# Kernel optimization log

Hardware: AMD Instinct MI355X
Metric: run time of the kernel (lower is better)

## Reference

```python
import jax, jax.numpy as jnp
import numpy as np

B, S, D, H = 2, 2048, 2048, 16
HD = D // H  # head_dim = 128
ROPE_BASE = 10000.0


def _rope_interleaved(x, cos, sin):
    # x: [B, S, H, HD]; cos/sin: [S, HD//2]
    xe = x[..., 0::2]
    xo = x[..., 1::2]
    c = cos[None, :, None, :]
    s = sin[None, :, None, :]
    oe = xe * c - xo * s
    oo = xe * s + xo * c
    # re-interleave pairs back to last dim
    return jnp.stack([oe, oo], axis=-1).reshape(x.shape)


def setup_inputs() -> dict:
    key = jax.random.key(0)
    k0, k1, k2, k3 = jax.random.split(key, 4)
    scale = D ** -0.5
    x = jax.random.normal(k0, (B, S, D), dtype=jnp.float32)
    wqk = jax.random.normal(k1, (2 * D, D), dtype=jnp.float32) * scale
    wv = jax.random.normal(k2, (D, D), dtype=jnp.float32) * scale
    wo = jax.random.normal(k3, (D, D), dtype=jnp.float32) * scale
    return {"x": x, "wqk": wqk, "wv": wv, "wo": wo}


def reference(x, wqk, wv, wo):
    b, s, d = x.shape
    # fused QK projection -> [B, S, 2, H, HD]
    xqk = (x @ wqk.T).reshape(b, s, 2, H, HD)
    xq = xqk[:, :, 0]
    xk = xqk[:, :, 1]
    xv = (x @ wv.T).reshape(b, s, H, HD)

    # interleaved rotary embedding (seqlen_offset=0, no-cache path)
    inv_freq = 1.0 / (ROPE_BASE ** (jnp.arange(0, HD, 2, dtype=jnp.float32) / HD))
    freqs = jnp.arange(s, dtype=jnp.float32)[:, None] * inv_freq[None, :]  # [S, HD//2]
    cos, sin = jnp.cos(freqs), jnp.sin(freqs)
    xq = _rope_interleaved(xq, cos, sin)
    xk = _rope_interleaved(xk, cos, sin)

    # causal scaled-dot-product attention
    scores = jnp.einsum("bqhd,bkhd->bhqk", xq, xk) * (HD ** -0.5)
    causal = jnp.tril(jnp.ones((s, s), dtype=bool))
    scores = jnp.where(causal[None, None], scores, jnp.finfo(scores.dtype).min)
    probs = jax.nn.softmax(scores, axis=-1)
    out = jnp.einsum("bhqk,bkhd->bqhd", probs, xv).reshape(b, s, d)
    return out @ wo.T
```

## Files before the change

kernel.cpp:

```cpp
#include <hip/hip_runtime.h>
#include <hip/hip_bf16.h>

#define NB 2
#define SEQ 2048
#define DMODEL 2048
#define NH 16
#define HD 128
#define QSCALE (0.08838834764831845f * 1.44269504088896f)
#define THRL2 11.5f

using bf16x8 = __attribute__((ext_vector_type(8))) __bf16;
using f32x4  = __attribute__((ext_vector_type(4))) float;

#define MFMA16 __builtin_amdgcn_mfma_f32_16x16x32_bf16

typedef __attribute__((address_space(1))) const void* gptr_t;
typedef __attribute__((address_space(3))) void* lptr_t;

__device__ inline void gload_lds16(const unsigned short* g, unsigned short* l) {
    __builtin_amdgcn_global_load_lds((gptr_t)g, (lptr_t)l, 16, 0, 0);
}

__device__ inline unsigned short f2b(float f) {
    unsigned u = __builtin_bit_cast(unsigned, f);
    u += 0x7FFF + ((u >> 16) & 1);
    return (unsigned short)(u >> 16);
}
__device__ inline float b2f(unsigned short h) {
    return __builtin_bit_cast(float, (unsigned)h << 16);
}
__device__ inline float fexp2(float x) {
    float r;
    asm("v_exp_f32 %0, %1" : "=v"(r) : "v"(x));
    return r;
}
__device__ inline unsigned cvtpk(float a, float b) {
    unsigned r;
    asm("v_cvt_pk_bf16_f32 %0, %1, %2" : "=v"(r) : "v"(a), "v"(b));
    return r;
}

__global__ void cast_f2b(const float* __restrict__ src, unsigned short* __restrict__ dst, int n) {
    int i = (blockIdx.x * 256 + threadIdx.x) * 4;
    if (i + 3 < n) {
        float4 v = *reinterpret_cast<const float4*>(src + i);
        ushort4 o;
        o.x = f2b(v.x); o.y = f2b(v.y); o.z = f2b(v.z); o.w = f2b(v.w);
        *reinterpret_cast<ushort4*>(dst + i) = o;
    }
}

template<int OUT_BF16>
__global__ __launch_bounds__(512) void gemm8p(const unsigned short* __restrict__ A,
                                              const unsigned short* __restrict__ Bw,
                                              void* __restrict__ Cout,
                                              int M, int N, int K) {
    __shared__ __align__(16) char lds[98304];
    int tid = threadIdx.x;
    int lane = tid & 63;
    int wid = tid >> 6;
    int wm = wid >> 2, wn = wid & 3;
    int row0 = blockIdx.y * 128;
    int col0 = blockIdx.x * 256;
    int lr = lane & 15, g = lane >> 4;

    const unsigned short* srcA[2];
    const unsigned short* srcB[4];
#pragma unroll
    for (int i = 0; i < 2; i++) {
        int chunk = i * 512 + tid;
        int ksub = chunk >> 9;
        int cw = chunk & 511;
        int row = cw >> 2, c = cw & 3;
        int cs = c ^ ((row >> 1) & 3);
        srcA[i] = A + (size_t)(row0 + row) * K + ksub * 32 + cs * 8;
    }
#pragma unroll
    for (int i = 0; i < 4; i++) {
        int chunk = i * 512 + tid;
        int ksub = chunk >> 10;
        int cw = chunk & 1023;
        int row = cw >> 2, c = cw & 3;
        int cs = c ^ ((row >> 1) & 3);
        srcB[i] = Bw + (size_t)(col0 + row) * K + ksub * 32 + cs * 8;
    }

    int offA[4][2], offB[4][2];
#pragma unroll
    for (int i = 0; i < 4; i++) {
        int row = wm * 64 + i * 16 + lr;
#pragma unroll
        for (int ks = 0; ks < 2; ks++)
            offA[i][ks] = ks * 8192 + row * 64 + ((g ^ ((row >> 1) & 3)) * 16);
    }
#pragma unroll
    for (int j = 0; j < 4; j++) {
        int row = wn * 64 + j * 16 + lr;
#pragma unroll
        for (int ks = 0; ks < 2; ks++)
            offB[j][ks] = ks * 16384 + row * 64 + ((g ^ ((row >> 1) & 3)) * 16);
    }

    f32x4 acc[4][4] = {};
    int NT = K >> 6;

#define STAGE8(t) {                                                                   \
        int kb_ = (t) * 64;                                                           \
        int bs_ = ((t) & 1) * 49152;                                                  \
        _Pragma("unroll")                                                             \
        for (int i_ = 0; i_ < 2; i_++)                                                \
            gload_lds16(srcA[i_] + kb_,                                               \
                (unsigned short*)(lds + bs_ + (i_ * 512 + (tid & ~63)) * 16));        \
        _Pragma("unroll")                                                             \
        for (int i_ = 0; i_ < 4; i_++)                                                \
            gload_lds16(srcB[i_] + kb_,                                               \
                (unsigned short*)(lds + bs_ + 16384 + (i_ * 512 + (tid & ~63)) * 16)); \
    }

    STAGE8(0);
    for (int t = 0; t < NT; ++t) {
        if (t + 1 < NT) {
            STAGE8(t + 1);
            asm volatile("s_waitcnt vmcnt(6)" ::: "memory");
        } else {
            asm volatile("s_waitcnt vmcnt(0)" ::: "memory");
        }
        __builtin_amdgcn_s_barrier();
        __builtin_amdgcn_sched_barrier(0);

        const char* ab = lds + (t & 1) * 49152;
        const char* bb = ab + 16384;

        bf16x8 b[4][2], a[2][2];
#pragma unroll
        for (int j = 0; j < 4; j++)
#pragma unroll
            for (int ks = 0; ks < 2; ks++)
                b[j][ks] = *reinterpret_cast<const bf16x8*>(bb + offB[j][ks]);
#pragma unroll
        for (int i = 0; i < 2; i++)
#pragma unroll
            for (int ks = 0; ks < 2; ks++)
                a[i][ks] = *reinterpret_cast<const bf16x8*>(ab + offA[i][ks]);
        asm volatile("s_waitcnt lgkmcnt(0)" ::: "memory");
        __builtin_amdgcn_sched_barrier(0);
        __builtin_amdgcn_s_setprio(1);
#pragma unroll
        for (int ks = 0; ks < 2; ks++)
#pragma unroll
            for (int i = 0; i < 2; i++)
#pragma unroll
                for (int j = 0; j < 4; j++)
                    acc[i][j] = MFMA16(a[i][ks], b[j][ks], acc[i][j], 0, 0, 0);
        __builtin_amdgcn_s_setprio(0);

        bf16x8 a2[2][2];
#pragma unroll
        for (int i = 0; i < 2; i++)
#pragma unroll
            for (int ks = 0; ks < 2; ks++)
                a2[i][ks] = *reinterpret_cast<const bf16x8*>(ab + offA[2 + i][ks]);
        asm volatile("s_waitcnt lgkmcnt(0)" ::: "memory");
        __builtin_amdgcn_sched_barrier(0);
        __builtin_amdgcn_s_barrier();
        __builtin_amdgcn_sched_barrier(0);
        __builtin_amdgcn_s_setprio(1);
#pragma unroll
        for (int ks = 0; ks < 2; ks++)
#pragma unroll
            for (int i = 0; i < 2; i++)
#pragma unroll
                for (int j = 0; j < 4; j++)
                    acc[2 + i][j] = MFMA16(a2[i][ks], b[j][ks], acc[2 + i][j], 0, 0, 0);
        __builtin_amdgcn_s_setprio(0);
    }
#undef STAGE8

    int orow = g * 4;
#pragma unroll
    for (int i = 0; i < 4; i++) {
#pragma unroll
        for (int j = 0; j < 4; j++) {
            int r0 = row0 + wm * 64 + i * 16 + orow;
            int c  = col0 + wn * 64 + j * 16 + lr;
#pragma unroll
            for (int r = 0; r < 4; r++) {
                float v = acc[i][j][r];
                if (OUT_BF16)
                    ((unsigned short*)Cout)[(size_t)(r0 + r) * N + c] = f2b(v);
                else
                    ((float*)Cout)[(size_t)(r0 + r) * N + c] = v;
            }
        }
    }
}

__global__ void rope_qk(const unsigned short* __restrict__ qkv,
                        unsigned short* __restrict__ qb,
                        unsigned short* __restrict__ kb) {
    int idx = blockIdx.x * 256 + threadIdx.x;
    int i = idx & 63;
    int h = (idx >> 6) & 15;
    int t = idx >> 10;
    int s = t & (SEQ - 1);
    int b = t >> 11;

    float inv = exp2f(-13.287712379549449f * (float)i * (1.0f / 64.0f));
    float ang = (float)s * inv;
    float sn, cs;
    sincosf(ang, &sn, &cs);

    const unsigned short* base = qkv + (size_t)t * 6144 + h * 128 + 2 * i;
    unsigned qv = *reinterpret_cast<const unsigned*>(base);
    unsigned kv = *reinterpret_cast<const unsigned*>(base + 2048);

    float qe = b2f((unsigned short)(qv & 0xFFFF));
    float qo = b2f((unsigned short)(qv >> 16));
    float ke = b2f((unsigned short)(kv & 0xFFFF));
    float ko = b2f((unsigned short)(kv >> 16));

    float qe2 = (qe * cs - qo * sn) * QSCALE;
    float qo2 = (qe * sn + qo * cs) * QSCALE;
    float ke2 = ke * cs - ko * sn;
    float ko2 = ke * sn + ko * cs;

    size_t o = ((size_t)(b * NH + h) * SEQ + s) * HD + 2 * i;
    *reinterpret_cast<unsigned*>(qb + o) = (unsigned)f2b(qe2) | ((unsigned)f2b(qo2) << 16);
    *reinterpret_cast<unsigned*>(kb + o) = (unsigned)f2b(ke2) | ((unsigned)f2b(ko2) << 16);
}

__global__ void v_rearr(const unsigned short* __restrict__ qkv, unsigned short* __restrict__ vt) {
    int idx = blockIdx.x * 256 + threadIdx.x;
    int s4 = (idx & 511) * 4;
    int d  = (idx >> 9) & 127;
    int h  = (idx >> 16) & 15;
    int b  = idx >> 20;
    ushort4 o;
    size_t rbase = (size_t)(b * SEQ + s4) * 6144 + 4096 + h * 128 + d;
    o.x = qkv[rbase];
    o.y = qkv[rbase + 6144];
    o.z = qkv[rbase + 2 * 6144];
    o.w = qkv[rbase + 3 * 6144];
    *reinterpret_cast<ushort4*>(vt + ((size_t)(b * NH + h) * HD + d) * SEQ + s4) = o;
}

__global__ __launch_bounds__(64, 1) void attn6(const unsigned short* __restrict__ Q,
                                               const unsigned short* __restrict__ Kb,
                                               const unsigned short* __restrict__ Vt,
                                               unsigned short* __restrict__ O) {
    __shared__ __align__(16) char lds[36864];

    int lane = threadIdx.x;
    int bid = blockIdx.x;
    int p  = bid >> 5;
    int bh = bid & 31;
    int lr = lane & 15;
    int g  = lane >> 4;
    int g4 = g * 4;
    int lk = g * 8;

    const unsigned short* Qp = Q  + (size_t)bh * SEQ * HD;
    const unsigned short* Kp = Kb + (size_t)bh * SEQ * HD;
    const unsigned short* Vp = Vt + (size_t)bh * HD * SEQ;
    char* pl = lds + 32768;
    int b = bh >> 4;
    int h = bh & 15;

    int srcoff[16];
#pragma unroll
    for (int i2 = 0; i2 < 16; ++i2) {
        int r = i2 * 4 + g;
        srcoff[i2] = r * HD + ((lr ^ (r & 7)) * 8);
    }

#define STAGEK(bufbase, kvbase)                                                     \
    {                                                                               \
        const unsigned short* kbase = Kp + (size_t)(kvbase) * HD;                   \
        _Pragma("unroll")                                                           \
        for (int i2 = 0; i2 < 16; ++i2)                                             \
            gload_lds16(kbase + srcoff[i2],                                         \
                        (unsigned short*)(lds + (bufbase) + i2 * 1024));            \
    }

    for (int ph = 0; ph < 2; ++ph) {
        int j  = ph ? (63 - p) : p;
        int q0 = j * 32;
        int ktiles = (j >> 1) + 1;

        bf16x8 qf[2][4];
#pragma unroll
        for (int f = 0; f < 2; f++)
#pragma unroll
            for (int kb = 0; kb < 4; kb++)
                qf[f][kb] = *reinterpret_cast<const bf16x8*>(Qp + (size_t)(q0 + f * 16 + lr) * HD + kb * 32 + lk);

        f32x4 oacc[2][8] = {};
        float m[2] = { -1e30f, -1e30f }, l[2] = { 0.0f, 0.0f };
        int qrow[2] = { q0 + lr, q0 + 16 + lr };

        STAGEK(0, 0);

        int cur = 0;
        for (int t = 0; t < ktiles; ++t) {
            int kv0 = t * 64;
            if (t + 1 < ktiles) {
                STAGEK((cur ^ 1) * 16384, kv0 + 64);
                asm volatile("s_waitcnt vmcnt(16)" ::: "memory");
            } else {
                asm volatile("s_waitcnt vmcnt(0)" ::: "memory");
            }
            __builtin_amdgcn_sched_barrier(0);

            char* kb_c = lds + cur * 16384;
            f32x4 s[2][4] = {};
#pragma unroll
            for (int kb = 0; kb < 4; kb++) {
#pragma unroll
                for (int jj = 0; jj < 4; jj++) {
                    int row = jj * 16 + lr;
                    int cin = ((kb * 4 + g) ^ (row & 7));
                    bf16x8 kf = *reinterpret_cast<const bf16x8*>(kb_c + row * 256 + cin * 16);
                    s[0][jj] = MFMA16(kf, qf[0][kb], s[0][jj], 0, 0, 0);
                    s[1][jj] = MFMA16(kf, qf[1][kb], s[1][jj], 0, 0, 0);
                }
            }

            bf16x8 vf[8][2];
#pragma unroll
            for (int db = 0; db < 8; db++)
#pragma unroll
                for (int ks = 0; ks < 2; ks++)
                    vf[db][ks] = *reinterpret_cast<const bf16x8*>(Vp + (size_t)(db * 16 + lr) * SEQ + kv0 + ks * 32 + lk);

#pragma unroll
            for (int f = 0; f < 2; f++) {
                int q = qrow[f];
                bool full = (kv0 + 63 <= q0 + f * 16);
                float mx = -1e30f;
                if (full) {
#pragma unroll
                    for (int jj = 0; jj < 4; jj++)
#pragma unroll
                        for (int r = 0; r < 4; r++)
                            mx = fmaxf(mx, s[f][jj][r]);
                } else {
#pragma unroll
                    for (int jj = 0; jj < 4; jj++)
#pragma unroll
                        for (int r = 0; r < 4; r++) {
                            int kv = kv0 + jj * 16 + g4 + r;
                            float v = (kv <= q) ? s[f][jj][r] : -1e30f;
                            s[f][jj][r] = v;
                            mx = fmaxf(mx, v);
                        }
                }
                mx = fmaxf(mx, __shfl_xor(mx, 16));
                mx = fmaxf(mx, __shfl_xor(mx, 32));

                if (!__all(mx <= m[f] + THRL2)) {
                    float mn = fmaxf(m[f], mx);
                    float sc = fexp2(m[f] - mn);
                    m[f] = mn;
                    l[f] *= sc;
#pragma unroll
                    for (int db = 0; db < 8; db++)
#pragma unroll
                        for (int r = 0; r < 4; r++)
                            oacc[f][db][r] *= sc;
                }

                int row = f * 16 + lr;
                int rb = row * 128;
                int sw = (row & 7) << 4;
                float rs = 0.0f;
#pragma unroll
                for (int jj = 0; jj < 4; jj++)
#pragma unroll
                    for (int hh = 0; hh < 2; hh++) {
                        float p0 = fexp2(s[f][jj][2 * hh]     - m[f]);
                        float p1 = fexp2(s[f][jj][2 * hh + 1] - m[f]);
                        rs += p0 + p1;
                        unsigned pk = cvtpk(p0, p1);
                        int colb = jj * 32 + g * 8 + 4 * hh;
                        *reinterpret_cast<unsigned*>(pl + rb + (colb ^ sw)) = pk;
                    }
                rs += __shfl_xor(rs, 16);
                rs += __shfl_xor(rs, 32);
                l[f] += rs;
            }

            asm volatile("s_waitcnt lgkmcnt(0)" ::: "memory");
            __builtin_amdgcn_sched_barrier(0);

            bf16x8 pb[2][2];
#pragma unroll
            for (int f = 0; f < 2; f++)
#pragma unroll
                for (int ks = 0; ks < 2; ks++) {
                    int row = f * 16 + lr;
                    int off = row * 128 + ((ks * 64 + g * 16) ^ ((row & 7) << 4));
                    pb[f][ks] = *reinterpret_cast<const bf16x8*>(pl + off);
                }
#pragma unroll
            for (int db = 0; db < 8; db++)
#pragma unroll
                for (int ks = 0; ks < 2; ks++) {
                    oacc[0][db] = MFMA16(vf[db][ks], pb[0][ks], oacc[0][db], 0, 0, 0);
                    oacc[1][db] = MFMA16(vf[db][ks], pb[1][ks], oacc[1][db], 0, 0, 0);
                }

            cur ^= 1;
        }

#pragma unroll
        for (int f = 0; f < 2; f++) {
            float inv = 1.0f / l[f];
            int q = q0 + f * 16 + lr;
            unsigned short* op = O + ((size_t)(b * SEQ + q)) * DMODEL + h * HD;
#pragma unroll
            for (int db = 0; db < 8; db++) {
                ushort4 o4;
                o4.x = f2b(oacc[f][db][0] * inv);
                o4.y = f2b(oacc[f][db][1] * inv);
                o4.z = f2b(oacc[f][db][2] * inv);
                o4.w = f2b(oacc[f][db][3] * inv);
                *reinterpret_cast<ushort4*>(op + db * 16 + g4) = o4;
            }
        }
    }
#undef STAGEK
}

extern "C" void kernel_launch(void* const* d_in, const int* in_sizes, int n_in,
                              void* d_out, int out_size, void* d_ws, size_t ws_size,
                              hipStream_t stream) {
    const float* x   = (const float*)d_in[0];
    const float* wqk = (const float*)d_in[1];
    const float* wv  = (const float*)d_in[2];
    const float* wo  = (const float*)d_in[3];

    unsigned short* xb  = (unsigned short*)d_ws;
    unsigned short* wb  = xb  + (size_t)8388608;
    unsigned short* qkv = wb  + (size_t)16777216;
    unsigned short* qb  = qkv + (size_t)25165824;
    unsigned short* kb  = qb  + (size_t)8388608;
    unsigned short* vt  = kb  + (size_t)8388608;
    unsigned short* ao  = vt  + (size_t)8388608;

    cast_f2b<<<8192, 256, 0, stream>>>(x,   xb, 8388608);
    cast_f2b<<<8192, 256, 0, stream>>>(wqk, wb, 8388608);
    cast_f2b<<<4096, 256, 0, stream>>>(wv,  wb + 8388608, 4194304);
    cast_f2b<<<4096, 256, 0, stream>>>(wo,  wb + 12582912, 4194304);

    gemm8p<1><<<dim3(24, 32), 512, 0, stream>>>(xb, wb, (void*)qkv, 4096, 6144, 2048);

    rope_qk<<<16384, 256, 0, stream>>>(qkv, qb, kb);
    v_rearr<<<8192, 256, 0, stream>>>(qkv, vt);

    attn6<<<1024, 64, 0, stream>>>(qb, kb, vt, ao);

    gemm8p<0><<<dim3(8, 32), 512, 0, stream>>>(ao, wb + 12582912, d_out, 4096, 2048, 2048);
}
```

Measured before the change: 316.6 us.

## Use 256x256-tile GEMM kernel with split-phase pipelining for QKV projection

Adds a new GEMM kernel with 256x256 output tiles (128 KB LDS, double-buffered, 8 waves each computing 128x64) and uses it for the fused QKV projection in place of the 128x256 tile kernel. The larger tile raises arithmetic intensity and cuts global/L2 traffic per FLOP. Loads for the next K-step are interleaved with MFMA phases and separated by barriers, with wave priority raised around the MFMA blocks. In exchange, the grid shrinks to 384 blocks with one block per CU because of the LDS size, and each thread holds more accumulator registers.

```diff
diff --git a/kernel.cpp b/kernel.cpp
--- a/kernel.cpp
+++ b/kernel.cpp
@@ -47,6 +47,170 @@
         ushort4 o;
         o.x = f2b(v.x); o.y = f2b(v.y); o.z = f2b(v.z); o.w = f2b(v.w);
         *reinterpret_cast<ushort4*>(dst + i) = o;
+    }
+}
+
+template<int OUT_BF16>
+__global__ __launch_bounds__(512) void gemm256(const unsigned short* __restrict__ A,
+                                               const unsigned short* __restrict__ Bw,
+                                               void* __restrict__ Cout,
+                                               int M, int N, int K) {
+    __shared__ __align__(16) char lds[131072];
+    int tid = threadIdx.x;
+    int lane = tid & 63;
+    int wid = tid >> 6;
+    int wm = wid >> 2, wn = wid & 3;
+    int row0 = blockIdx.y * 256;
+    int col0 = blockIdx.x * 256;
+    int lr = lane & 15, g = lane >> 4;
+
+    const unsigned short *pA[2], *pB[2];
+    int ldsc[2];
+#pragma unroll
+    for (int i = 0; i < 2; i++) {
+        int chunk = i * 512 + tid;
+        int row = chunk >> 2, c = chunk & 3;
+        int cs = c ^ ((row >> 1) & 3);
+        pA[i] = A  + (size_t)(row0 + row) * K + cs * 8;
+        pB[i] = Bw + (size_t)(col0 + row) * K + cs * 8;
+        ldsc[i] = (i * 512 + (tid & ~63)) * 16;
+    }
+
+#define STAGE_A(bufb, kbase, h)  {                                                    \
+        _Pragma("unroll")                                                             \
+        for (int i_ = 0; i_ < 2; i_++)                                                \
+            gload_lds16(pA[i_] + (kbase) + (h) * 32,                                  \
+                (unsigned short*)(lds + (bufb) + (h) * 16384 + ldsc[i_]));            \
+    }
+#define STAGE_B(bufb, kbase, h)  {                                                    \
+        _Pragma("unroll")                                                             \
+        for (int i_ = 0; i_ < 2; i_++)                                                \
+            gload_lds16(pB[i_] + (kbase) + (h) * 32,                                  \
+                (unsigned short*)(lds + (bufb) + 32768 + (h) * 16384 + ldsc[i_]));    \
+    }
+
+    int offA[8][2], offB[4][2];
+#pragma unroll
+    for (int i = 0; i < 8; i++) {
+        int row = wm * 128 + i * 16 + lr;
+#pragma unroll
+        for (int ks = 0; ks < 2; ks++)
+            offA[i][ks] = ks * 16384 + row * 64 + ((g ^ ((row >> 1) & 3)) * 16);
+    }
+#pragma unroll
+    for (int j = 0; j < 4; j++) {
+        int row = wn * 64 + j * 16 + lr;
+#pragma unroll
+        for (int ks = 0; ks < 2; ks++)
+            offB[j][ks] = 32768 + ks * 16384 + row * 64 + ((g ^ ((row >> 1) & 3)) * 16);
+    }
+
+    f32x4 acc[8][4] = {};
+    int NT = K >> 6;
+
+    STAGE_A(0, 0, 0); STAGE_B(0, 0, 0); STAGE_A(0, 0, 1); STAGE_B(0, 0, 1);
+    asm volatile("s_waitcnt vmcnt(4)" ::: "memory");
+    __builtin_amdgcn_s_barrier();
+    __builtin_amdgcn_sched_barrier(0);
+
+    for (int t = 0; t < NT; ++t) {
+        const char* bufc = lds + (t & 1) * 65536;
+        int bufn = ((t + 1) & 1) * 65536;
+        bool hn = (t + 1 < NT);
+        int kn = (t + 1) * 64;
+
+        bf16x8 av[4], bv[4];
+
+#pragma unroll
+        for (int j = 0; j < 4; j++) bv[j] = *reinterpret_cast<const bf16x8*>(bufc + offB[j][0]);
+#pragma unroll
+        for (int i = 0; i < 4; i++) av[i] = *reinterpret_cast<const bf16x8*>(bufc + offA[i][0]);
+        if (hn) STAGE_A(bufn, kn, 0);
+        __builtin_amdgcn_s_barrier();
+        asm volatile("s_waitcnt lgkmcnt(0)" ::: "memory");
+        __builtin_amdgcn_sched_barrier(0);
+        __builtin_amdgcn_s_setprio(1);
+#pragma unroll
+        for (int i = 0; i < 4; i++)
+#pragma unroll
+            for (int j = 0; j < 4; j++)
+                acc[i][j] = MFMA16(av[i], bv[j], acc[i][j], 0, 0, 0);
+        __builtin_amdgcn_s_setprio(0);
+        __builtin_amdgcn_s_barrier();
+        __builtin_amdgcn_sched_barrier(0);
+
+#pragma unroll
+        for (int i = 0; i < 4; i++) av[i] = *reinterpret_cast<const bf16x8*>(bufc + offA[4 + i][0]);
+        if (hn) STAGE_B(bufn, kn, 0);
+        __builtin_amdgcn_s_barrier();
+        asm volatile("s_waitcnt lgkmcnt(0)" ::: "memory");
+        __builtin_amdgcn_sched_barrier(0);
+        __builtin_amdgcn_s_setprio(1);
+#pragma unroll
+        for (int i = 0; i < 4; i++)
+#pragma unroll
+            for (int j = 0; j < 4; j++)
+                acc[4 + i][j] = MFMA16(av[i], bv[j], acc[4 + i][j], 0, 0, 0);
+        __builtin_amdgcn_s_setprio(0);
+        if (hn) asm volatile("s_waitcnt vmcnt(4)" ::: "memory");
+        else    asm volatile("s_waitcnt vmcnt(0)" ::: "memory");
+        __builtin_amdgcn_s_barrier();
+        __builtin_amdgcn_sched_barrier(0);
+
+#pragma unroll
+        for (int j = 0; j < 4; j++) bv[j] = *reinterpret_cast<const bf16x8*>(bufc + offB[j][1]);
+#pragma unroll
+        for (int i = 0; i < 4; i++) av[i] = *reinterpret_cast<const bf16x8*>(bufc + offA[i][1]);
+        if (hn) STAGE_A(bufn, kn, 1);
+        __builtin_amdgcn_s_barrier();
+        asm volatile("s_waitcnt lgkmcnt(0)" ::: "memory");
+        __builtin_amdgcn_sched_barrier(0);
+        __builtin_amdgcn_s_setprio(1);
+#pragma unroll
+        for (int i = 0; i < 4; i++)
+#pragma unroll
+            for (int j = 0; j < 4; j++)
+                acc[i][j] = MFMA16(av[i], bv[j], acc[i][j], 0, 0, 0);
+        __builtin_amdgcn_s_setprio(0);
+        __builtin_amdgcn_s_barrier();
+        __builtin_amdgcn_sched_barrier(0);
+
+#pragma unroll
+        for (int i = 0; i < 4; i++) av[i] = *reinterpret_cast<const bf16x8*>(bufc + offA[4 + i][1]);
+        if (hn) STAGE_B(bufn, kn, 1);
+        __builtin_amdgcn_s_barrier();
+        asm volatile("s_waitcnt lgkmcnt(0)" ::: "memory");
+        __builtin_amdgcn_sched_barrier(0);
+        __builtin_amdgcn_s_setprio(1);
+#pragma unroll
+        for (int i = 0; i < 4; i++)
+#pragma unroll
+            for (int j = 0; j < 4; j++)
+                acc[4 + i][j] = MFMA16(av[i], bv[j], acc[4 + i][j], 0, 0, 0);
+        __builtin_amdgcn_s_setprio(0);
+        if (hn) asm volatile("s_waitcnt vmcnt(4)" ::: "memory");
+        __builtin_amdgcn_s_barrier();
+        __builtin_amdgcn_sched_barrier(0);
+    }
+#undef STAGE_A
+#undef STAGE_B
+
+    int orow = g * 4;
+#pragma unroll
+    for (int i = 0; i < 8; i++) {
+#pragma unroll
+        for (int j = 0; j < 4; j++) {
+            int r0 = row0 + wm * 128 + i * 16 + orow;
+            int c  = col0 + wn * 64 + j * 16 + lr;
+#pragma unroll
+            for (int r = 0; r < 4; r++) {
+                float v = acc[i][j][r];
+                if (OUT_BF16)
+                    ((unsigned short*)Cout)[(size_t)(r0 + r) * N + c] = f2b(v);
+                else
+                    ((float*)Cout)[(size_t)(r0 + r) * N + c] = v;
+            }
+        }
     }
 }
 
@@ -452,7 +616,7 @@
     cast_f2b<<<4096, 256, 0, stream>>>(wv,  wb + 8388608, 4194304);
     cast_f2b<<<4096, 256, 0, stream>>>(wo,  wb + 12582912, 4194304);
 
-    gemm8p<1><<<dim3(24, 32), 512, 0, stream>>>(xb, wb, (void*)qkv, 4096, 6144, 2048);
+    gemm256<1><<<dim3(24, 16), 512, 0, stream>>>(xb, wb, (void*)qkv, 4096, 6144, 2048);
 
     rope_qk<<<16384, 256, 0, stream>>>(qkv, qb, kb);
     v_rearr<<<8192, 256, 0, stream>>>(qkv, vt);
```

Measured after the change: 332.0 us. 1.05x slower.

## Split KV tiles across two waves per query tile with LDS merge

Applied to the files above, without the earlier changes.

Replaces the single-wave attention kernel, which processed a paired short and long query tile in sequence, with a two-wave block per query tile. Each wave handles alternating KV tiles with its own K buffer and P scratch, and the two partial softmax states are merged through LDS at the end. The grid doubles to 2048 blocks and blocks are issued longest-first. This aims to raise parallelism and shorten the serial KV loop, at the cost of losing the double-buffered K prefetch within a wave and adding a merge step with barriers.

```diff
diff --git a/kernel.cpp b/kernel.cpp
--- a/kernel.cpp
+++ b/kernel.cpp
@@ -244,16 +244,20 @@
     *reinterpret_cast<ushort4*>(vt + ((size_t)(b * NH + h) * HD + d) * SEQ + s4) = o;
 }
 
-__global__ __launch_bounds__(64, 1) void attn6(const unsigned short* __restrict__ Q,
-                                               const unsigned short* __restrict__ Kb,
-                                               const unsigned short* __restrict__ Vt,
-                                               unsigned short* __restrict__ O) {
-    __shared__ __align__(16) char lds[36864];
-
-    int lane = threadIdx.x;
+__global__ __launch_bounds__(128, 1) void attn7(const unsigned short* __restrict__ Q,
+                                                const unsigned short* __restrict__ Kb,
+                                                const unsigned short* __restrict__ Vt,
+                                                unsigned short* __restrict__ O) {
+    __shared__ __align__(16) char lds[40960];
+
+    int tid = threadIdx.x;
+    int lane = tid & 63;
+    int w = tid >> 6;
     int bid = blockIdx.x;
-    int p  = bid >> 5;
+    int qt = 63 - (bid >> 5);
     int bh = bid & 31;
+    int q0 = qt * 32;
+    int ktiles = (qt >> 1) + 1;
     int lr = lane & 15;
     int g  = lane >> 4;
     int g4 = g * 4;
@@ -262,7 +266,8 @@
     const unsigned short* Qp = Q  + (size_t)bh * SEQ * HD;
     const unsigned short* Kp = Kb + (size_t)bh * SEQ * HD;
     const unsigned short* Vp = Vt + (size_t)bh * HD * SEQ;
-    char* pl = lds + 32768;
+    char* kl = lds + w * 16384;
+    char* pl = lds + 32768 + w * 4096;
     int b = bh >> 4;
     int h = bh & 15;
 
@@ -273,162 +278,167 @@
         srcoff[i2] = r * HD + ((lr ^ (r & 7)) * 8);
     }
 
-#define STAGEK(bufbase, kvbase)                                                     \
-    {                                                                               \
+#define STAGEK7(kvbase) {                                                           \
         const unsigned short* kbase = Kp + (size_t)(kvbase) * HD;                   \
         _Pragma("unroll")                                                           \
         for (int i2 = 0; i2 < 16; ++i2)                                             \
             gload_lds16(kbase + srcoff[i2],                                         \
-                        (unsigned short*)(lds + (bufbase) + i2 * 1024));            \
-    }
-
-    for (int ph = 0; ph < 2; ++ph) {
-        int j  = ph ? (63 - p) : p;
-        int q0 = j * 32;
-        int ktiles = (j >> 1) + 1;
-
-        bf16x8 qf[2][4];
+                        (unsigned short*)(kl + i2 * 1024));                         \
+    }
+
+    bf16x8 qf[2][4];
+#pragma unroll
+    for (int f = 0; f < 2; f++)
+#pragma unroll
+        for (int kb = 0; kb < 4; kb++)
+            qf[f][kb] = *reinterpret_cast<const bf16x8*>(Qp + (size_t)(q0 + f * 16 + lr) * HD + kb * 32 + lk);
+
+    f32x4 oacc[2][8] = {};
+    float m[2] = { -1e30f, -1e30f }, l[2] = { 0.0f, 0.0f };
+    int qrow[2] = { q0 + lr, q0 + 16 + lr };
+
+    if (w < ktiles) STAGEK7(w * 64);
+
+    for (int t = w; t < ktiles; t += 2) {
+        int kv0 = t * 64;
+        asm volatile("s_waitcnt vmcnt(0)" ::: "memory");
+        __builtin_amdgcn_sched_barrier(0);
+
+        f32x4 s[2][4] = {};
+#pragma unroll
+        for (int kb = 0; kb < 4; kb++) {
+#pragma unroll
+            for (int jj = 0; jj < 4; jj++) {
+                int row = jj * 16 + lr;
+                int cin = ((kb * 4 + g) ^ (row & 7));
+                bf16x8 kf = *reinterpret_cast<const bf16x8*>(kl + row * 256 + cin * 16);
+                s[0][jj] = MFMA16(kf, qf[0][kb], s[0][jj], 0, 0, 0);
+                s[1][jj] = MFMA16(kf, qf[1][kb], s[1][jj], 0, 0, 0);
+            }
+        }
+
+        bf16x8 vf[8][2];
+#pragma unroll
+        for (int db = 0; db < 8; db++)
+#pragma unroll
+            for (int ks = 0; ks < 2; ks++)
+                vf[db][ks] = *reinterpret_cast<const bf16x8*>(Vp + (size_t)(db * 16 + lr) * SEQ + kv0 + ks * 32 + lk);
+
+#pragma unroll
+        for (int f = 0; f < 2; f++) {
+            int q = qrow[f];
+            bool full = (kv0 + 63 <= q0 + f * 16);
+            float mx = -1e30f;
+            if (full) {
+#pragma unroll
+                for (int jj = 0; jj < 4; jj++)
+#pragma unroll
+                    for (int r = 0; r < 4; r++)
+                        mx = fmaxf(mx, s[f][jj][r]);
+            } else {
+#pragma unroll
+                for (int jj = 0; jj < 4; jj++)
+#pragma unroll
+                    for (int r = 0; r < 4; r++) {
+                        int kv = kv0 + jj * 16 + g4 + r;
+                        float v = (kv <= q) ? s[f][jj][r] : -1e30f;
+                        s[f][jj][r] = v;
+                        mx = fmaxf(mx, v);
+                    }
+            }
+            mx = fmaxf(mx, __shfl_xor(mx, 16));
+            mx = fmaxf(mx, __shfl_xor(mx, 32));
+
+            if (!__all(mx <= m[f] + THRL2)) {
+                float mn = fmaxf(m[f], mx);
+                float sc = fexp2(m[f] - mn);
+                m[f] = mn;
+                l[f] *= sc;
+#pragma unroll
+                for (int db = 0; db < 8; db++)
+#pragma unroll
+                    for (int r = 0; r < 4; r++)
+                        oacc[f][db][r] *= sc;
+            }
+
+            int row = f * 16 + lr;
+            int rb = row * 128;
+            int sw = (row & 7) << 4;
+            float rs = 0.0f;
+#pragma unroll
+            for (int jj = 0; jj < 4; jj++)
+#pragma unroll
+                for (int hh = 0; hh < 2; hh++) {
+                    float p0 = fexp2(s[f][jj][2 * hh]     - m[f]);
+                    float p1 = fexp2(s[f][jj][2 * hh + 1] - m[f]);
+                    rs += p0 + p1;
+                    unsigned pk = cvtpk(p0, p1);
+                    int colb = jj * 32 + g * 8 + 4 * hh;
+                    *reinterpret_cast<unsigned*>(pl + rb + (colb ^ sw)) = pk;
+                }
+            rs += __shfl_xor(rs, 16);
+            rs += __shfl_xor(rs, 32);
+            l[f] += rs;
+        }
+
+        asm volatile("s_waitcnt lgkmcnt(0)" ::: "memory");
+        __builtin_amdgcn_sched_barrier(0);
+
+        if (t + 2 < ktiles) STAGEK7((t + 2) * 64);
+
+        bf16x8 pb[2][2];
 #pragma unroll
         for (int f = 0; f < 2; f++)
 #pragma unroll
-            for (int kb = 0; kb < 4; kb++)
-                qf[f][kb] = *reinterpret_cast<const bf16x8*>(Qp + (size_t)(q0 + f * 16 + lr) * HD + kb * 32 + lk);
-
-        f32x4 oacc[2][8] = {};
-        float m[2] = { -1e30f, -1e30f }, l[2] = { 0.0f, 0.0f };
-        int qrow[2] = { q0 + lr, q0 + 16 + lr };
-
-        STAGEK(0, 0);
-
-        int cur = 0;
-        for (int t = 0; t < ktiles; ++t) {
-            int kv0 = t * 64;
-            if (t + 1 < ktiles) {
-                STAGEK((cur ^ 1) * 16384, kv0 + 64);
-                asm volatile("s_waitcnt vmcnt(16)" ::: "memory");
-            } else {
-                asm volatile("s_waitcnt vmcnt(0)" ::: "memory");
-            }
-            __builtin_amdgcn_sched_barrier(0);
-
-            char* kb_c = lds + cur * 16384;
-            f32x4 s[2][4] = {};
-#pragma unroll
-            for (int kb = 0; kb < 4; kb++) {
-#pragma unroll
-                for (int jj = 0; jj < 4; jj++) {
-                    int row = jj * 16 + lr;
-                    int cin = ((kb * 4 + g) ^ (row & 7));
-                    bf16x8 kf = *reinterpret_cast<const bf16x8*>(kb_c + row * 256 + cin * 16);
-                    s[0][jj] = MFMA16(kf, qf[0][kb], s[0][jj], 0, 0, 0);
-                    s[1][jj] = MFMA16(kf, qf[1][kb], s[1][jj], 0, 0, 0);
-                }
-            }
-
-            bf16x8 vf[8][2];
+            for (int ks = 0; ks < 2; ks++) {
+                int row = f * 16 + lr;
+                int off = row * 128 + ((ks * 64 + g * 16) ^ ((row & 7) << 4));
+                pb[f][ks] = *reinterpret_cast<const bf16x8*>(pl + off);
+            }
+#pragma unroll
+        for (int db = 0; db < 8; db++)
+#pragma unroll
+            for (int ks = 0; ks < 2; ks++) {
+                oacc[0][db] = MFMA16(vf[db][ks], pb[0][ks], oacc[0][db], 0, 0, 0);
+                oacc[1][db] = MFMA16(vf[db][ks], pb[1][ks], oacc[1][db], 0, 0, 0);
+            }
+    }
+#undef STAGEK7
+
+    __syncthreads();
+    if (w == 1) {
+#pragma unroll
+        for (int f = 0; f < 2; f++) {
 #pragma unroll
             for (int db = 0; db < 8; db++)
-#pragma unroll
-                for (int ks = 0; ks < 2; ks++)
-                    vf[db][ks] = *reinterpret_cast<const bf16x8*>(Vp + (size_t)(db * 16 + lr) * SEQ + kv0 + ks * 32 + lk);
-
-#pragma unroll
-            for (int f = 0; f < 2; f++) {
-                int q = qrow[f];
-                bool full = (kv0 + 63 <= q0 + f * 16);
-                float mx = -1e30f;
-                if (full) {
-#pragma unroll
-                    for (int jj = 0; jj < 4; jj++)
-#pragma unroll
-                        for (int r = 0; r < 4; r++)
-                            mx = fmaxf(mx, s[f][jj][r]);
-                } else {
-#pragma unroll
-                    for (int jj = 0; jj < 4; jj++)
-#pragma unroll
-                        for (int r = 0; r < 4; r++) {
-                            int kv = kv0 + jj * 16 + g4 + r;
-                            float v = (kv <= q) ? s[f][jj][r] : -1e30f;
-                            s[f][jj][r] = v;
-                            mx = fmaxf(mx, v);
-                        }
-                }
-                mx = fmaxf(mx, __shfl_xor(mx, 16));
-                mx = fmaxf(mx, __shfl_xor(mx, 32));
-
-                if (!__all(mx <= m[f] + THRL2)) {
-                    float mn = fmaxf(m[f], mx);
-                    float sc = fexp2(m[f] - mn);
-                    m[f] = mn;
-                    l[f] *= sc;
-#pragma unroll
-                    for (int db = 0; db < 8; db++)
-#pragma unroll
-                        for (int r = 0; r < 4; r++)
-                            oacc[f][db][r] *= sc;
-                }
-
-                int row = f * 16 + lr;
-                int rb = row * 128;
-                int sw = (row & 7) << 4;
-                float rs = 0.0f;
-#pragma unroll
-                for (int jj = 0; jj < 4; jj++)
-#pragma unroll
-                    for (int hh = 0; hh < 2; hh++) {
-                        float p0 = fexp2(s[f][jj][2 * hh]     - m[f]);
-                        float p1 = fexp2(s[f][jj][2 * hh + 1] - m[f]);
-                        rs += p0 + p1;
-                        unsigned pk = cvtpk(p0, p1);
-                        int colb = jj * 32 + g * 8 + 4 * hh;
-                        *reinterpret_cast<unsigned*>(pl + rb + (colb ^ sw)) = pk;
-                    }
-                rs += __shfl_xor(rs, 16);
-                rs += __shfl_xor(rs, 32);
-                l[f] += rs;
-            }
-
-            asm volatile("s_waitcnt lgkmcnt(0)" ::: "memory");
-            __builtin_amdgcn_sched_barrier(0);
-
-            bf16x8 pb[2][2];
-#pragma unroll
-            for (int f = 0; f < 2; f++)
-#pragma unroll
-                for (int ks = 0; ks < 2; ks++) {
-                    int row = f * 16 + lr;
-                    int off = row * 128 + ((ks * 64 + g * 16) ^ ((row & 7) << 4));
-                    pb[f][ks] = *reinterpret_cast<const bf16x8*>(pl + off);
-                }
-#pragma unroll
-            for (int db = 0; db < 8; db++)
-#pragma unroll
-                for (int ks = 0; ks < 2; ks++) {
-                    oacc[0][db] = MFMA16(vf[db][ks], pb[0][ks], oacc[0][db], 0, 0, 0);
-                    oacc[1][db] = MFMA16(vf[db][ks], pb[1][ks], oacc[1][db], 0, 0, 0);
-                }
-
-            cur ^= 1;
-        }
-
+                *reinterpret_cast<f32x4*>(lds + ((f * 8 + db) * 64 + lane) * 16) = oacc[f][db];
+            *reinterpret_cast<float2*>(lds + 16384 + (f * 64 + lane) * 8) = make_float2(m[f], l[f]);
+        }
+    }
+    __syncthreads();
+    if (w == 0) {
 #pragma unroll
         for (int f = 0; f < 2; f++) {
-            float inv = 1.0f / l[f];
+            float2 ml1 = *reinterpret_cast<const float2*>(lds + 16384 + (f * 64 + lane) * 8);
+            float mt = fmaxf(m[f], ml1.x);
+            float sc0 = fexp2(m[f] - mt);
+            float sc1 = fexp2(ml1.x - mt);
+            float L = l[f] * sc0 + ml1.y * sc1;
+            float inv = 1.0f / L;
             int q = q0 + f * 16 + lr;
             unsigned short* op = O + ((size_t)(b * SEQ + q)) * DMODEL + h * HD;
 #pragma unroll
             for (int db = 0; db < 8; db++) {
+                f32x4 o1 = *reinterpret_cast<const f32x4*>(lds + ((f * 8 + db) * 64 + lane) * 16);
                 ushort4 o4;
-                o4.x = f2b(oacc[f][db][0] * inv);
-                o4.y = f2b(oacc[f][db][1] * inv);
-                o4.z = f2b(oacc[f][db][2] * inv);
-                o4.w = f2b(oacc[f][db][3] * inv);
+                o4.x = f2b((oacc[f][db][0] * sc0 + o1[0] * sc1) * inv);
+                o4.y = f2b((oacc[f][db][1] * sc0 + o1[1] * sc1) * inv);
+                o4.z = f2b((oacc[f][db][2] * sc0 + o1[2] * sc1) * inv);
+                o4.w = f2b((oacc[f][db][3] * sc0 + o1[3] * sc1) * inv);
                 *reinterpret_cast<ushort4*>(op + db * 16 + g4) = o4;
             }
         }
     }
-#undef STAGEK
 }
 
 extern "C" void kernel_launch(void* const* d_in, const int* in_sizes, int n_in,
@@ -457,7 +467,7 @@
     rope_qk<<<16384, 256, 0, stream>>>(qkv, qb, kb);
     v_rearr<<<8192, 256, 0, stream>>>(qkv, vt);
 
-    attn6<<<1024, 64, 0, stream>>>(qb, kb, vt, ao);
+    attn7<<<2048, 128, 0, stream>>>(qb, kb, vt, ao);
 
     gemm8p<0><<<dim3(8, 32), 512, 0, stream>>>(ao, wb + 12582912, d_out, 4096, 2048, 2048);
 }
```

Measured after the change: 326.2 us. 3.0% more time.

## Fuse RoPE and head-major Q/K scatter into QKV GEMM epilogue, tile V transpose

Applied to the files above, without the earlier changes.

The QKV projection GEMM epilogue now applies the rotary embedding, using a precomputed cos/sin table and a lane shuffle to fetch the pair partner, and writes Q (pre-scaled) and K straight into head-major bf16 buffers. This removes the separate rope_qk kernel and the round trip of the full QKV intermediate. V is written row-major and transposed by a new LDS-tiled kernel, replacing the strided per-element gather. The cost is a more complex epilogue with scattered 2-byte stores and table loads, plus one extra small kernel to build the table.

```diff
diff --git a/kernel.cpp b/kernel.cpp
--- a/kernel.cpp
+++ b/kernel.cpp
@@ -50,10 +50,25 @@
     }
 }
 
-template<int OUT_BF16>
+__global__ void rope_tab(float2* __restrict__ tab) {
+    int idx = blockIdx.x * 256 + threadIdx.x;
+    int i = idx & 63;
+    int s = idx >> 6;
+    float inv = exp2f(-13.287712379549449f * (float)i * (1.0f / 64.0f));
+    float ang = (float)s * inv;
+    float sn, cs;
+    sincosf(ang, &sn, &cs);
+    tab[idx] = make_float2(cs, sn);
+}
+
+template<int MODE>
 __global__ __launch_bounds__(512) void gemm8p(const unsigned short* __restrict__ A,
                                               const unsigned short* __restrict__ Bw,
                                               void* __restrict__ Cout,
+                                              unsigned short* __restrict__ qb,
+                                              unsigned short* __restrict__ kbp,
+                                              unsigned short* __restrict__ vx,
+                                              const float2* __restrict__ tab,
                                               int M, int N, int K) {
     __shared__ __align__(16) char lds[98304];
     int tid = threadIdx.x;
@@ -177,71 +192,87 @@
 #undef STAGE8
 
     int orow = g * 4;
-#pragma unroll
-    for (int i = 0; i < 4; i++) {
-#pragma unroll
-        for (int j = 0; j < 4; j++) {
-            int r0 = row0 + wm * 64 + i * 16 + orow;
-            int c  = col0 + wn * 64 + j * 16 + lr;
-#pragma unroll
-            for (int r = 0; r < 4; r++) {
-                float v = acc[i][j][r];
-                if (OUT_BF16)
-                    ((unsigned short*)Cout)[(size_t)(r0 + r) * N + c] = f2b(v);
-                else
-                    ((float*)Cout)[(size_t)(r0 + r) * N + c] = v;
+    if (MODE == 0) {
+#pragma unroll
+        for (int i = 0; i < 4; i++) {
+#pragma unroll
+            for (int j = 0; j < 4; j++) {
+                int r0 = row0 + wm * 64 + i * 16 + orow;
+                int c  = col0 + wn * 64 + j * 16 + lr;
+#pragma unroll
+                for (int r = 0; r < 4; r++)
+                    ((float*)Cout)[(size_t)(r0 + r) * N + c] = acc[i][j][r];
             }
         }
-    }
-}
-
-__global__ void rope_qk(const unsigned short* __restrict__ qkv,
-                        unsigned short* __restrict__ qb,
-                        unsigned short* __restrict__ kb) {
-    int idx = blockIdx.x * 256 + threadIdx.x;
-    int i = idx & 63;
-    int h = (idx >> 6) & 15;
-    int t = idx >> 10;
-    int s = t & (SEQ - 1);
-    int b = t >> 11;
-
-    float inv = exp2f(-13.287712379549449f * (float)i * (1.0f / 64.0f));
-    float ang = (float)s * inv;
-    float sn, cs;
-    sincosf(ang, &sn, &cs);
-
-    const unsigned short* base = qkv + (size_t)t * 6144 + h * 128 + 2 * i;
-    unsigned qv = *reinterpret_cast<const unsigned*>(base);
-    unsigned kv = *reinterpret_cast<const unsigned*>(base + 2048);
-
-    float qe = b2f((unsigned short)(qv & 0xFFFF));
-    float qo = b2f((unsigned short)(qv >> 16));
-    float ke = b2f((unsigned short)(kv & 0xFFFF));
-    float ko = b2f((unsigned short)(kv >> 16));
-
-    float qe2 = (qe * cs - qo * sn) * QSCALE;
-    float qo2 = (qe * sn + qo * cs) * QSCALE;
-    float ke2 = ke * cs - ko * sn;
-    float ko2 = ke * sn + ko * cs;
-
-    size_t o = ((size_t)(b * NH + h) * SEQ + s) * HD + 2 * i;
-    *reinterpret_cast<unsigned*>(qb + o) = (unsigned)f2b(qe2) | ((unsigned)f2b(qo2) << 16);
-    *reinterpret_cast<unsigned*>(kb + o) = (unsigned)f2b(ke2) | ((unsigned)f2b(ko2) << 16);
-}
-
-__global__ void v_rearr(const unsigned short* __restrict__ qkv, unsigned short* __restrict__ vt) {
-    int idx = blockIdx.x * 256 + threadIdx.x;
-    int s4 = (idx & 511) * 4;
-    int d  = (idx >> 9) & 127;
-    int h  = (idx >> 16) & 15;
-    int b  = idx >> 20;
-    ushort4 o;
-    size_t rbase = (size_t)(b * SEQ + s4) * 6144 + 4096 + h * 128 + d;
-    o.x = qkv[rbase];
-    o.y = qkv[rbase + 6144];
-    o.z = qkv[rbase + 2 * 6144];
-    o.w = qkv[rbase + 3 * 6144];
-    *reinterpret_cast<ushort4*>(vt + ((size_t)(b * NH + h) * HD + d) * SEQ + s4) = o;
+    } else {
+        int bx = blockIdx.x;
+        if (bx < 16) {
+            const bool isQ = (bx < 8);
+            unsigned short* dst = isQ ? qb : kbp;
+#pragma unroll
+            for (int i = 0; i < 4; i++) {
+#pragma unroll
+                for (int j = 0; j < 4; j++) {
+                    int c = col0 + wn * 64 + j * 16 + lr;
+                    int cc = c & 2047;
+                    int h = cc >> 7, d = cc & 127, i2 = d >> 1;
+                    int odd = lr & 1;
+#pragma unroll
+                    for (int r = 0; r < 4; r++) {
+                        int trow = row0 + wm * 64 + i * 16 + orow + r;
+                        int s = trow & (SEQ - 1), bb2 = trow >> 11;
+                        float v = acc[i][j][r];
+                        float pv = __shfl_xor(v, 1);
+                        float2 cssn = tab[s * 64 + i2];
+                        float out = odd ? (pv * cssn.y + v * cssn.x)
+                                        : (v * cssn.x - pv * cssn.y);
+                        if (isQ) out *= QSCALE;
+                        dst[((size_t)((bb2 * NH + h) * SEQ + s)) * HD + d] = f2b(out);
+                    }
+                }
+            }
+        } else {
+#pragma unroll
+            for (int i = 0; i < 4; i++) {
+#pragma unroll
+                for (int j = 0; j < 4; j++) {
+                    int cc = col0 + wn * 64 + j * 16 + lr - 4096;
+#pragma unroll
+                    for (int r = 0; r < 4; r++) {
+                        int trow = row0 + wm * 64 + i * 16 + orow + r;
+                        vx[(size_t)trow * 2048 + cc] = f2b(acc[i][j][r]);
+                    }
+                }
+            }
+        }
+    }
+}
+
+__global__ __launch_bounds__(256) void v_tr(const unsigned short* __restrict__ vx,
+                                            unsigned short* __restrict__ vt) {
+    __shared__ unsigned short tl[64][68];
+    int bid = blockIdx.x;
+    int st = bid & 31;
+    int dt = (bid >> 5) & 1;
+    int bh = bid >> 6;
+    int b = bh >> 4, h = bh & 15;
+    int tid = threadIdx.x;
+    int rr = tid >> 2;
+    int rc = (tid & 3) * 16;
+
+    const unsigned short* src = vx + (size_t)(b * SEQ + st * 64 + rr) * 2048 + h * HD + dt * 64 + rc;
+    uint4 v0 = *reinterpret_cast<const uint4*>(src);
+    uint4 v1 = *reinterpret_cast<const uint4*>(src + 8);
+    *reinterpret_cast<uint4*>(&tl[rr][rc]) = v0;
+    *reinterpret_cast<uint4*>(&tl[rr][rc + 8]) = v1;
+    __syncthreads();
+
+    unsigned short tmp[16];
+#pragma unroll
+    for (int k = 0; k < 16; k++) tmp[k] = tl[rc + k][rr];
+    unsigned short* dst = vt + (size_t)(bh * HD + dt * 64 + rr) * SEQ + st * 64 + rc;
+    *reinterpret_cast<uint4*>(dst)     = *reinterpret_cast<const uint4*>(&tmp[0]);
+    *reinterpret_cast<uint4*>(dst + 8) = *reinterpret_cast<const uint4*>(&tmp[8]);
 }
 
 __global__ __launch_bounds__(64, 1) void attn6(const unsigned short* __restrict__ Q,
@@ -441,23 +472,24 @@
 
     unsigned short* xb  = (unsigned short*)d_ws;
     unsigned short* wb  = xb  + (size_t)8388608;
-    unsigned short* qkv = wb  + (size_t)16777216;
-    unsigned short* qb  = qkv + (size_t)25165824;
+    unsigned short* qb  = wb  + (size_t)16777216;
     unsigned short* kb  = qb  + (size_t)8388608;
-    unsigned short* vt  = kb  + (size_t)8388608;
+    unsigned short* vx  = kb  + (size_t)8388608;
+    unsigned short* vt  = vx  + (size_t)8388608;
     unsigned short* ao  = vt  + (size_t)8388608;
+    float2* tab = (float2*)(ao + (size_t)8388608);
 
     cast_f2b<<<8192, 256, 0, stream>>>(x,   xb, 8388608);
     cast_f2b<<<8192, 256, 0, stream>>>(wqk, wb, 8388608);
     cast_f2b<<<4096, 256, 0, stream>>>(wv,  wb + 8388608, 4194304);
     cast_f2b<<<4096, 256, 0, stream>>>(wo,  wb + 12582912, 4194304);
-
-    gemm8p<1><<<dim3(24, 32), 512, 0, stream>>>(xb, wb, (void*)qkv, 4096, 6144, 2048);
-
-    rope_qk<<<16384, 256, 0, stream>>>(qkv, qb, kb);
-    v_rearr<<<8192, 256, 0, stream>>>(qkv, vt);
+    rope_tab<<<512, 256, 0, stream>>>(tab);
+
+    gemm8p<2><<<dim3(24, 32), 512, 0, stream>>>(xb, wb, nullptr, qb, kb, vx, tab, 4096, 6144, 2048);
+
+    v_tr<<<2048, 256, 0, stream>>>(vx, vt);
 
     attn6<<<1024, 64, 0, stream>>>(qb, kb, vt, ao);
 
-    gemm8p<0><<<dim3(8, 32), 512, 0, stream>>>(ao, wb + 12582912, d_out, 4096, 2048, 2048);
-}
+    gemm8p<0><<<dim3(8, 32), 512, 0, stream>>>(ao, wb + 12582912, d_out, nullptr, nullptr, nullptr, nullptr, 4096, 2048, 2048);
+}
```

Result: faster. 283.2 us (-10.5%).
